# Optimization experiments

Hardware: AMD Instinct MI355X
Metric: run time of the kernel (lower is better)

The kernel has to match this reference:

```python
import jax, jax.numpy as jnp
import numpy as np

N_NODES = 100000
N_EDGES = 3200000
NEG_SLOPE = 0.2  # PyG GATConv default
EPS = 1e-16      # PyG softmax denominator guard


def setup_inputs() -> dict:
    key = jax.random.key(0)
    ks = jax.random.split(key, 12)
    x = jax.random.normal(ks[0], (N_NODES, 4), dtype=jnp.float32)
    edge_index = jax.random.randint(ks[1], (2, N_EDGES), 0, N_NODES, dtype=jnp.int32)
    # conv1: in=4, heads=4, out=16, concat -> 64
    W1 = jax.random.normal(ks[2], (4, 64), dtype=jnp.float32) * 0.5
    a_src1 = jax.random.normal(ks[3], (4, 16), dtype=jnp.float32) * 0.3
    a_dst1 = jax.random.normal(ks[4], (4, 16), dtype=jnp.float32) * 0.3
    b1 = jnp.zeros((64,), dtype=jnp.float32)
    # conv2: in=64, heads=1, out=2, no concat
    W2 = jax.random.normal(ks[5], (64, 2), dtype=jnp.float32) * 0.2
    a_src2 = jax.random.normal(ks[6], (1, 2), dtype=jnp.float32) * 0.3
    a_dst2 = jax.random.normal(ks[7], (1, 2), dtype=jnp.float32) * 0.3
    b2 = jnp.zeros((2,), dtype=jnp.float32)
    return dict(x=x, edge_index=edge_index, W1=W1, a_src1=a_src1, a_dst1=a_dst1,
                b1=b1, W2=W2, a_src2=a_src2, a_dst2=a_dst2, b2=b2)


def _gat_layer(h_in, src, dst, W, a_s, a_d, b, heads, out_dim, concat):
    n = h_in.shape[0]
    h = (h_in @ W).reshape(n, heads, out_dim)            # [N, H, F]
    alpha_s = jnp.einsum('nhf,hf->nh', h, a_s)           # [N, H]
    alpha_d = jnp.einsum('nhf,hf->nh', h, a_d)
    e = jax.nn.leaky_relu(alpha_s[src] + alpha_d[dst], NEG_SLOPE)  # [E, H]
    # segment softmax over incoming edges of each dst node
    m = jax.ops.segment_max(e, dst, num_segments=n)      # [N, H]
    e = jnp.exp(e - m[dst])
    s = jax.ops.segment_sum(e, dst, num_segments=n)
    alpha = e / (s[dst] + EPS)                            # [E, H]
    msg = h[src] * alpha[:, :, None]                      # [E, H, F]
    out = jax.ops.segment_sum(msg, dst, num_segments=n)   # [N, H, F]
    if concat:
        out = out.reshape(n, heads * out_dim)
    else:
        out = out.mean(axis=1)
    return out + b


def reference(x, edge_index, W1, a_src1, a_dst1, b1, W2, a_src2, a_dst2, b2):
    n = x.shape[0]
    loop = jnp.arange(n, dtype=edge_index.dtype)
    src = jnp.concatenate([edge_index[0], loop])  # PyG add_self_loops=True
    dst = jnp.concatenate([edge_index[1], loop])
    h = jax.nn.elu(_gat_layer(x, src, dst, W1, a_src1, a_dst1, b1, 4, 16, True))
    h = _gat_layer(h, src, dst, W2, a_src2, a_dst2, b2, 1, 2, False)
    return jax.nn.log_softmax(h, axis=1)
```

## Files before the change

kernel.cpp:

```cpp
#include <hip/hip_runtime.h>
#include <hip/hip_fp16.h>
#include <math.h>

#define NEG_SLOPE 0.2f
#define EPS_F 1e-16f

#define P1_NB 256
#define P1S_THREADS 1024
#define LOCAL_BITS 7
#define NLOCAL 128
#define MAX_BEDGES 5632
#define SCAN_SHIFT 11

__device__ __forceinline__ float leaky(float v) {
    return v >= 0.f ? v : NEG_SLOPE * v;
}

__global__ void k_phaseA(const float* __restrict__ x, const float* __restrict__ W1,
                         const float* __restrict__ a_src1, const float* __restrict__ a_dst1,
                         __half* __restrict__ h1h, float* __restrict__ as1,
                         float* __restrict__ ad1, int N) {
    int node = blockIdx.x * 4 + (threadIdx.x >> 6);
    if (node >= N) return;
    int lane = threadIdx.x & 63;
    float x0 = x[node * 4 + 0], x1 = x[node * 4 + 1];
    float x2 = x[node * 4 + 2], x3 = x[node * 4 + 3];
    float h = x0 * W1[lane] + x1 * W1[64 + lane] + x2 * W1[128 + lane] + x3 * W1[192 + lane];
    h1h[(size_t)node * 64 + lane] = __float2half(h);
    float as = h * a_src1[lane];
    float ad = h * a_dst1[lane];
#pragma unroll
    for (int m = 8; m >= 1; m >>= 1) {
        as += __shfl_xor(as, m, 16);
        ad += __shfl_xor(ad, m, 16);
    }
    if ((lane & 15) == 0) {
        int head = lane >> 4;
        as1[node * 4 + head] = as;
        ad1[node * 4 + head] = ad;
    }
}

__global__ void k_p1hist(const int* __restrict__ dst, int* __restrict__ histT,
                         int E, int chunk, int nbucket) {
    __shared__ int cnt[1024];
    int blk = blockIdx.x, t = threadIdx.x;
    for (int i = t; i < nbucket; i += P1S_THREADS) cnt[i] = 0;
    __syncthreads();
    int s = blk * chunk, e = min(E, s + chunk);
    for (int i = s + t; i < e; i += P1S_THREADS)
        atomicAdd(&cnt[dst[i] >> LOCAL_BITS], 1);
    __syncthreads();
    for (int i = t; i < nbucket; i += P1S_THREADS)
        histT[i * P1_NB + blk] = cnt[i];
}

__global__ void k_scan1(const int* __restrict__ in, int* __restrict__ out,
                        int* __restrict__ blockSums, int M) {
    __shared__ int sdata[256];
    int t = threadIdx.x;
    int base = blockIdx.x * 2048 + t * 8;
    int v[8];
    int total = 0;
#pragma unroll
    for (int k = 0; k < 8; ++k) {
        int idx = base + k;
        v[k] = (idx < M) ? in[idx] : 0;
        total += v[k];
    }
    sdata[t] = total;
    __syncthreads();
    for (int off = 1; off < 256; off <<= 1) {
        int x = (t >= off) ? sdata[t - off] : 0;
        __syncthreads();
        sdata[t] += x;
        __syncthreads();
    }
    int run = sdata[t] - total;
#pragma unroll
    for (int k = 0; k < 8; ++k) {
        int idx = base + k;
        if (idx < M) out[idx] = run;
        run += v[k];
    }
    if (t == 255) blockSums[blockIdx.x] = sdata[255];
}

__global__ void k_scan2(int* __restrict__ bs, int n) {
    __shared__ int s[128];
    int t = threadIdx.x;
    int v = (t < n) ? bs[t] : 0;
    s[t] = v;
    __syncthreads();
    for (int o = 1; o < 128; o <<= 1) {
        int x = (t >= o) ? s[t - o] : 0;
        __syncthreads();
        s[t] += x;
        __syncthreads();
    }
    if (t < n) bs[t] = s[t] - v;
}

__global__ void k_p1scatter(const int* __restrict__ src, const int* __restrict__ dst,
                            const int* __restrict__ baseT, const int* __restrict__ bsScan,
                            unsigned int* __restrict__ packed,
                            int E, int chunk, int nbucket) {
    __shared__ int cnt[1024];
    int blk = blockIdx.x, t = threadIdx.x;
    for (int i = t; i < nbucket; i += P1S_THREADS) {
        int idx = i * P1_NB + blk;
        cnt[i] = baseT[idx] + bsScan[idx >> SCAN_SHIFT];
    }
    __syncthreads();
    int s = blk * chunk, e = min(E, s + chunk);
    for (int i = s + t; i < e; i += P1S_THREADS) {
        int d = dst[i];
        int pos = atomicAdd(&cnt[d >> LOCAL_BITS], 1);
        packed[pos] = ((unsigned int)(d & (NLOCAL - 1)) << 23) | (unsigned int)src[i];
    }
}

__global__ void k_fineL1(const unsigned int* __restrict__ packed, const int* __restrict__ baseT,
                         const int* __restrict__ bsScan,
                         const __half* __restrict__ h1h, const float* __restrict__ as1,
                         const float* __restrict__ ad1, const float* __restrict__ b1,
                         const float* __restrict__ W2, const float* __restrict__ a_src2,
                         const float* __restrict__ a_dst2,
                         int* __restrict__ csr, int* __restrict__ rowptr,
                         uint2* __restrict__ node2, int N, int E) {
    __shared__ int cnt[NLOCAL];
    __shared__ int off[NLOCAL];
    __shared__ int cur[NLOCAL];
    __shared__ unsigned int eb[MAX_BEDGES];

    int b = blockIdx.x, t = threadIdx.x;
    int nbucket = gridDim.x;

    int i0 = b * P1_NB;
    int startE = baseT[i0] + bsScan[i0 >> SCAN_SHIFT];
    int endE = E;
    if (b != nbucket - 1) {
        int i1 = (b + 1) * P1_NB;
        endE = baseT[i1] + bsScan[i1 >> SCAN_SHIFT];
    }
    int ne = endE - startE;
    if (ne > MAX_BEDGES) ne = MAX_BEDGES;

    if (t < NLOCAL) cnt[t] = 0;
    __syncthreads();
    for (int i = t; i < ne; i += 1024)
        atomicAdd(&cnt[packed[startE + i] >> 23], 1);
    __syncthreads();
    if (t < NLOCAL) cur[t] = cnt[t];
    __syncthreads();
    for (int o = 1; o < NLOCAL; o <<= 1) {
        int v = (t < NLOCAL && t >= o) ? cur[t - o] : 0;
        __syncthreads();
        if (t < NLOCAL) cur[t] += v;
        __syncthreads();
    }
    if (t < NLOCAL) {
        int excl = cur[t] - cnt[t];
        off[t] = excl;
        int node = (b << LOCAL_BITS) + t;
        if (node < N) rowptr[node] = startE + excl;
    }
    if (b == 0 && t == 0) rowptr[N] = E;
    __syncthreads();
    if (t < NLOCAL) cur[t] = off[t];
    __syncthreads();
    for (int i = t; i < ne; i += 1024) {
        unsigned int p = packed[startE + i];
        int pos = atomicAdd(&cur[p >> 23], 1);
        eb[pos] = p;
    }
    __syncthreads();
    for (int i = t; i < ne; i += 1024)
        csr[startE + i] = (int)(eb[i] & 0x7FFFFFu);

    int wave = t >> 6;
    int lane = t & 63;
    int head4 = lane & 3;
    int j     = lane >> 2;
    int sub   = lane >> 4;
    int fl    = lane & 15;
    int h     = fl >> 2;
    int nodeBase = b << LOCAL_BITS;

    for (int q = 0; q < 8; ++q) {
        int local = wave * 8 + q;
        int node = nodeBase + local;
        if (node >= N) break;
        int beg = off[local];
        int end = beg + cnt[local];

        float ad_s1 = ad1[node * 4 + head4];
        float pself4 = __expf(leaky(as1[node * 4 + head4] + ad_s1));
        float psum = (lane < 4) ? pself4 : 0.f;

        float pselfF = __shfl(pself4, h);
        float a0 = 0.f, a1 = 0.f, a2 = 0.f, a3 = 0.f;
        if (sub == 0) {
            float2 raw = *(const float2*)(h1h + ((size_t)node << 6) + (fl << 2));
            __half2 h01 = *reinterpret_cast<__half2*>(&raw.x);
            __half2 h23 = *reinterpret_cast<__half2*>(&raw.y);
            float2 f01 = __half22float2(h01), f23 = __half22float2(h23);
            a0 = pselfF * f01.x; a1 = pselfF * f01.y;
            a2 = pselfF * f23.x; a3 = pselfF * f23.y;
        }

        for (int c = beg; c < end; c += 16) {
            int e = c + j;
            bool valid = e < end;
            int s = (int)(eb[valid ? e : beg] & 0x7FFFFFu);
            float v = leaky(as1[s * 4 + head4] + ad_s1);
            float p = valid ? __expf(v) : 0.f;
            psum += p;

            int s_q[4];
#pragma unroll
            for (int m = 0; m < 4; ++m) s_q[m] = __shfl(s, m * 16 + sub * 4);
            float2 raw[4];
#pragma unroll
            for (int m = 0; m < 4; ++m)
                raw[m] = *(const float2*)(h1h + ((size_t)s_q[m] << 6) + (fl << 2));
            float p_q[4];
#pragma unroll
            for (int m = 0; m < 4; ++m) p_q[m] = __shfl(p, m * 16 + sub * 4 + h);
#pragma unroll
            for (int m = 0; m < 4; ++m) {
                __half2 h01 = *reinterpret_cast<__half2*>(&raw[m].x);
                __half2 h23 = *reinterpret_cast<__half2*>(&raw[m].y);
                float2 f01 = __half22float2(h01), f23 = __half22float2(h23);
                a0 = fmaf(p_q[m], f01.x, a0);
                a1 = fmaf(p_q[m], f01.y, a1);
                a2 = fmaf(p_q[m], f23.x, a2);
                a3 = fmaf(p_q[m], f23.y, a3);
            }
        }

        a0 += __shfl_xor(a0, 16); a0 += __shfl_xor(a0, 32);
        a1 += __shfl_xor(a1, 16); a1 += __shfl_xor(a1, 32);
        a2 += __shfl_xor(a2, 16); a2 += __shfl_xor(a2, 32);
        a3 += __shfl_xor(a3, 16); a3 += __shfl_xor(a3, 32);

#pragma unroll
        for (int m = 4; m <= 32; m <<= 1) psum += __shfl_xor(psum, m);
        float psumF = __shfl(psum, h);
        float inv = 1.f / (psumF + EPS_F);

        float4 b1v = ((const float4*)b1)[fl];
        float o0 = a0 * inv + b1v.x;
        float o1 = a1 * inv + b1v.y;
        float o2 = a2 * inv + b1v.z;
        float o3 = a3 * inv + b1v.w;
        float e0 = o0 > 0.f ? o0 : (__expf(o0) - 1.f);
        float e1 = o1 > 0.f ? o1 : (__expf(o1) - 1.f);
        float e2 = o2 > 0.f ? o2 : (__expf(o2) - 1.f);
        float e3 = o3 > 0.f ? o3 : (__expf(o3) - 1.f);

        float4 w01 = ((const float4*)W2)[fl * 2];
        float4 w23 = ((const float4*)W2)[fl * 2 + 1];
        float c0 = e0 * w01.x + e1 * w01.z + e2 * w23.x + e3 * w23.z;
        float c1 = e0 * w01.y + e1 * w01.w + e2 * w23.y + e3 * w23.w;
#pragma unroll
        for (int m = 8; m >= 1; m >>= 1) {
            c0 += __shfl_xor(c0, m);
            c1 += __shfl_xor(c1, m);
        }
        if (lane == 0) {
            float as2 = c0 * a_src2[0] + c1 * a_src2[1];
            float ad2 = c0 * a_dst2[0] + c1 * a_dst2[1];
            __half2 hc = __floats2half2_rn(c0, c1);
            __half2 ha = __floats2half2_rn(as2, ad2);
            node2[node] = make_uint2(*(unsigned int*)&hc, *(unsigned int*)&ha);
        }
    }
}

__global__ void k_layer2(const int* __restrict__ rowptr, const int* __restrict__ csr,
                         const uint2* __restrict__ node2, const float* __restrict__ b2,
                         float* __restrict__ out, int N) {
    int node = blockIdx.x * 16 + (threadIdx.x >> 4);
    if (node >= N) return;
    int sl = threadIdx.x & 15;

    uint2 mraw = node2[node];
    __half2 mch = *reinterpret_cast<__half2*>(&mraw.x);
    __half2 mah = *reinterpret_cast<__half2*>(&mraw.y);
    float2 mc = __half22float2(mch);
    float2 ma = __half22float2(mah);
    float ad = ma.y;
    int beg = rowptr[node], end = rowptr[node + 1];

    float psum = 0.f, a0 = 0.f, a1 = 0.f;
    for (int e = beg + sl; e < end; e += 16) {
        uint2 sraw = node2[csr[e]];
        __half2 sch = *reinterpret_cast<__half2*>(&sraw.x);
        __half2 sah = *reinterpret_cast<__half2*>(&sraw.y);
        float2 sc = __half22float2(sch);
        float2 sa = __half22float2(sah);
        float p = __expf(leaky(sa.x + ad));
        psum += p;
        a0 = fmaf(p, sc.x, a0);
        a1 = fmaf(p, sc.y, a1);
    }
    if (sl == 0) {
        float p = __expf(leaky(ma.x + ad));
        psum += p;
        a0 = fmaf(p, mc.x, a0);
        a1 = fmaf(p, mc.y, a1);
    }
#pragma unroll
    for (int m = 8; m >= 1; m >>= 1) {
        psum += __shfl_xor(psum, m);
        a0 += __shfl_xor(a0, m);
        a1 += __shfl_xor(a1, m);
    }
    if (sl == 0) {
        float inv = 1.f / (psum + EPS_F);
        float o0 = a0 * inv + b2[0];
        float o1 = a1 * inv + b2[1];
        float mx = fmaxf(o0, o1);
        float lse = mx + logf(__expf(o0 - mx) + __expf(o1 - mx));
        out[node * 2 + 0] = o0 - lse;
        out[node * 2 + 1] = o1 - lse;
    }
}


extern "C" void kernel_launch(void* const* d_in, const int* in_sizes, int n_in,
                              void* d_out, int out_size, void* d_ws, size_t ws_size,
                              hipStream_t stream) {
    const float* x      = (const float*)d_in[0];
    const int*   ei     = (const int*)d_in[1];
    const float* W1     = (const float*)d_in[2];
    const float* a_src1 = (const float*)d_in[3];
    const float* a_dst1 = (const float*)d_in[4];
    const float* b1     = (const float*)d_in[5];
    const float* W2     = (const float*)d_in[6];
    const float* a_src2 = (const float*)d_in[7];
    const float* a_dst2 = (const float*)d_in[8];
    const float* b2     = (const float*)d_in[9];
    float* out = (float*)d_out;

    int N = in_sizes[0] / 4;
    int E = in_sizes[1] / 2;
    const int* e_src = ei;
    const int* e_dst = ei + E;

    int nbucket = (N + NLOCAL - 1) >> LOCAL_BITS;
    int M = nbucket * P1_NB;

    char* w = (char*)d_ws;
    auto alloc = [&](size_t bytes) -> void* {
        void* p = (void*)w;
        w += (bytes + 255) & ~(size_t)255;
        return p;
    };
    __half* h1h       = (__half*)alloc((size_t)N * 64 * 2);
    float*  as1       = (float*)alloc((size_t)N * 4 * 4);
    float*  ad1       = (float*)alloc((size_t)N * 4 * 4);
    uint2*  node2     = (uint2*)alloc((size_t)N * 8);
    int*    rowptr    = (int*)alloc((size_t)(N + 1) * 4);
    int*    histT     = (int*)alloc((size_t)M * 4);
    int*    baseT     = (int*)alloc((size_t)M * 4);
    int*    blockSums = (int*)alloc(256 * 4);
    int*    csr       = (int*)alloc((size_t)E * 4);
    unsigned int* packed = (unsigned int*)alloc((size_t)E * 4);

    int chunk = (E + P1_NB - 1) / P1_NB;
    int nbScan = (M + 2047) / 2048;
    int nodeb = (N + 3) / 4;

    k_phaseA<<<nodeb, 256, 0, stream>>>(x, W1, a_src1, a_dst1, h1h, as1, ad1, N);
    k_p1hist<<<P1_NB, P1S_THREADS, 0, stream>>>(e_dst, histT, E, chunk, nbucket);
    k_scan1<<<nbScan, 256, 0, stream>>>(histT, baseT, blockSums, M);
    k_scan2<<<1, 128, 0, stream>>>(blockSums, nbScan);
    k_p1scatter<<<P1_NB, P1S_THREADS, 0, stream>>>(e_src, e_dst, baseT, blockSums,
                                                   packed, E, chunk, nbucket);
    k_fineL1<<<nbucket, 1024, 0, stream>>>(packed, baseT, blockSums,
                                           h1h, as1, ad1, b1, W2,
                                           a_src2, a_dst2, csr, rowptr, node2, N, E);
    k_layer2<<<(N + 15) / 16, 256, 0, stream>>>(rowptr, csr, node2, b2, out, N);
}
```

Measured before the change: 252.6 us.

## Fuse node projection into scatter kernel and cache bucket edges in registers

The standalone layer-1 projection kernel is folded into the edge scatter kernel as extra blocks, which removes one launch and lets the projection run alongside the scatter. In the fine CSR build, each thread loads its packed edges once into registers and reuses them for both the counting pass and the placement pass, so packed is no longer read from global memory twice. The leaky ReLU becomes a fmaxf. Register caching assumes at most 6144 edges per bucket, while the existing shared buffer cap is 5632, and the larger fused kernel may lower occupancy.

```diff
diff --git a/kernel.cpp b/kernel.cpp
--- a/kernel.cpp
+++ b/kernel.cpp
@@ -10,35 +10,11 @@
 #define LOCAL_BITS 7
 #define NLOCAL 128
 #define MAX_BEDGES 5632
+#define REGS_PB 6
 #define SCAN_SHIFT 11
 
 __device__ __forceinline__ float leaky(float v) {
-    return v >= 0.f ? v : NEG_SLOPE * v;
-}
-
-__global__ void k_phaseA(const float* __restrict__ x, const float* __restrict__ W1,
-                         const float* __restrict__ a_src1, const float* __restrict__ a_dst1,
-                         __half* __restrict__ h1h, float* __restrict__ as1,
-                         float* __restrict__ ad1, int N) {
-    int node = blockIdx.x * 4 + (threadIdx.x >> 6);
-    if (node >= N) return;
-    int lane = threadIdx.x & 63;
-    float x0 = x[node * 4 + 0], x1 = x[node * 4 + 1];
-    float x2 = x[node * 4 + 2], x3 = x[node * 4 + 3];
-    float h = x0 * W1[lane] + x1 * W1[64 + lane] + x2 * W1[128 + lane] + x3 * W1[192 + lane];
-    h1h[(size_t)node * 64 + lane] = __float2half(h);
-    float as = h * a_src1[lane];
-    float ad = h * a_dst1[lane];
-#pragma unroll
-    for (int m = 8; m >= 1; m >>= 1) {
-        as += __shfl_xor(as, m, 16);
-        ad += __shfl_xor(ad, m, 16);
-    }
-    if ((lane & 15) == 0) {
-        int head = lane >> 4;
-        as1[node * 4 + head] = as;
-        ad1[node * 4 + head] = ad;
-    }
+    return fmaxf(v, NEG_SLOPE * v);
 }
 
 __global__ void k_p1hist(const int* __restrict__ dst, int* __restrict__ histT,
@@ -101,22 +77,48 @@
     if (t < n) bs[t] = s[t] - v;
 }
 
-__global__ void k_p1scatter(const int* __restrict__ src, const int* __restrict__ dst,
-                            const int* __restrict__ baseT, const int* __restrict__ bsScan,
-                            unsigned int* __restrict__ packed,
-                            int E, int chunk, int nbucket) {
+__global__ void __launch_bounds__(1024)
+k_scatterA(const int* __restrict__ src, const int* __restrict__ dst,
+           const int* __restrict__ baseT, const int* __restrict__ bsScan,
+           unsigned int* __restrict__ packed, int E, int chunk, int nbucket,
+           const float* __restrict__ x, const float* __restrict__ W1,
+           const float* __restrict__ a_src1, const float* __restrict__ a_dst1,
+           __half* __restrict__ h1h, float* __restrict__ as1,
+           float* __restrict__ ad1, int N) {
     __shared__ int cnt[1024];
     int blk = blockIdx.x, t = threadIdx.x;
-    for (int i = t; i < nbucket; i += P1S_THREADS) {
-        int idx = i * P1_NB + blk;
-        cnt[i] = baseT[idx] + bsScan[idx >> SCAN_SHIFT];
-    }
-    __syncthreads();
-    int s = blk * chunk, e = min(E, s + chunk);
-    for (int i = s + t; i < e; i += P1S_THREADS) {
-        int d = dst[i];
-        int pos = atomicAdd(&cnt[d >> LOCAL_BITS], 1);
-        packed[pos] = ((unsigned int)(d & (NLOCAL - 1)) << 23) | (unsigned int)src[i];
+    if (blk < P1_NB) {
+        for (int i = t; i < nbucket; i += P1S_THREADS) {
+            int idx = i * P1_NB + blk;
+            cnt[i] = baseT[idx] + bsScan[idx >> SCAN_SHIFT];
+        }
+        __syncthreads();
+        int s = blk * chunk, e = min(E, s + chunk);
+        for (int i = s + t; i < e; i += P1S_THREADS) {
+            int d = dst[i];
+            int pos = atomicAdd(&cnt[d >> LOCAL_BITS], 1);
+            packed[pos] = ((unsigned int)(d & (NLOCAL - 1)) << 23) | (unsigned int)src[i];
+        }
+    } else {
+        int node = (blk - P1_NB) * 16 + (t >> 6);
+        if (node >= N) return;
+        int lane = t & 63;
+        float4 xv = ((const float4*)x)[node];
+        float h = xv.x * W1[lane] + xv.y * W1[64 + lane] +
+                  xv.z * W1[128 + lane] + xv.w * W1[192 + lane];
+        h1h[(size_t)node * 64 + lane] = __float2half(h);
+        float as = h * a_src1[lane];
+        float ad = h * a_dst1[lane];
+#pragma unroll
+        for (int m = 8; m >= 1; m >>= 1) {
+            as += __shfl_xor(as, m, 16);
+            ad += __shfl_xor(ad, m, 16);
+        }
+        if ((lane & 15) == 0) {
+            int head = lane >> 4;
+            as1[node * 4 + head] = as;
+            ad1[node * 4 + head] = ad;
+        }
     }
 }
 
@@ -135,6 +137,7 @@
 
     int b = blockIdx.x, t = threadIdx.x;
     int nbucket = gridDim.x;
+    int nodeBase = b << LOCAL_BITS;
 
     int i0 = b * P1_NB;
     int startE = baseT[i0] + bsScan[i0 >> SCAN_SHIFT];
@@ -148,8 +151,16 @@
 
     if (t < NLOCAL) cnt[t] = 0;
     __syncthreads();
-    for (int i = t; i < ne; i += 1024)
-        atomicAdd(&cnt[packed[startE + i] >> 23], 1);
+
+    unsigned int pk[REGS_PB];
+#pragma unroll
+    for (int k = 0; k < REGS_PB; ++k) {
+        int i = t + k * 1024;
+        pk[k] = (i < ne) ? packed[startE + i] : 0xFFFFFFFFu;
+    }
+#pragma unroll
+    for (int k = 0; k < REGS_PB; ++k)
+        if (pk[k] != 0xFFFFFFFFu) atomicAdd(&cnt[pk[k] >> 23], 1);
     __syncthreads();
     if (t < NLOCAL) cur[t] = cnt[t];
     __syncthreads();
@@ -162,18 +173,19 @@
     if (t < NLOCAL) {
         int excl = cur[t] - cnt[t];
         off[t] = excl;
-        int node = (b << LOCAL_BITS) + t;
+        int node = nodeBase + t;
         if (node < N) rowptr[node] = startE + excl;
     }
     if (b == 0 && t == 0) rowptr[N] = E;
     __syncthreads();
     if (t < NLOCAL) cur[t] = off[t];
     __syncthreads();
-    for (int i = t; i < ne; i += 1024) {
-        unsigned int p = packed[startE + i];
-        int pos = atomicAdd(&cur[p >> 23], 1);
-        eb[pos] = p;
-    }
+#pragma unroll
+    for (int k = 0; k < REGS_PB; ++k)
+        if (pk[k] != 0xFFFFFFFFu) {
+            int pos = atomicAdd(&cur[pk[k] >> 23], 1);
+            eb[pos] = pk[k];
+        }
     __syncthreads();
     for (int i = t; i < ne; i += 1024)
         csr[startE + i] = (int)(eb[i] & 0x7FFFFFu);
@@ -185,7 +197,6 @@
     int sub   = lane >> 4;
     int fl    = lane & 15;
     int h     = fl >> 2;
-    int nodeBase = b << LOCAL_BITS;
 
     for (int q = 0; q < 8; ++q) {
         int local = wave * 8 + q;
@@ -371,16 +382,16 @@
 
     int chunk = (E + P1_NB - 1) / P1_NB;
     int nbScan = (M + 2047) / 2048;
-    int nodeb = (N + 3) / 4;
-
-    k_phaseA<<<nodeb, 256, 0, stream>>>(x, W1, a_src1, a_dst1, h1h, as1, ad1, N);
+    int nodeb16 = (N + 15) / 16;
+
     k_p1hist<<<P1_NB, P1S_THREADS, 0, stream>>>(e_dst, histT, E, chunk, nbucket);
     k_scan1<<<nbScan, 256, 0, stream>>>(histT, baseT, blockSums, M);
     k_scan2<<<1, 128, 0, stream>>>(blockSums, nbScan);
-    k_p1scatter<<<P1_NB, P1S_THREADS, 0, stream>>>(e_src, e_dst, baseT, blockSums,
-                                                   packed, E, chunk, nbucket);
+    k_scatterA<<<P1_NB + nodeb16, P1S_THREADS, 0, stream>>>(
+        e_src, e_dst, baseT, blockSums, packed, E, chunk, nbucket,
+        x, W1, a_src1, a_dst1, h1h, as1, ad1, N);
     k_fineL1<<<nbucket, 1024, 0, stream>>>(packed, baseT, blockSums,
                                            h1h, as1, ad1, b1, W2,
                                            a_src2, a_dst2, csr, rowptr, node2, N, E);
-    k_layer2<<<(N + 15) / 16, 256, 0, stream>>>(rowptr, csr, node2, b2, out, N);
-}
+    k_layer2<<<nodeb16, 256, 0, stream>>>(rowptr, csr, node2, b2, out, N);
+}
```

Result: faster. 241.1 us (-4.6%).
